# Optimization experiments

Measured on AMD Instinct MI355X. Metric: run time of the kernel, lower is better.

## Reference

```python
import jax, jax.numpy as jnp
import numpy as np

BATCH, SEQ_LEN, VEC_DIM, WIDTH = 64, 256, 512, 3


def setup_inputs() -> dict:
    key = jax.random.key(0)
    k = jax.random.split(key, 8)
    F0r = jax.random.normal(k[0], (BATCH, SEQ_LEN, VEC_DIM), jnp.float32)
    F1r = jax.random.normal(k[1], (BATCH, SEQ_LEN, VEC_DIM), jnp.float32)
    sent0_mask = (jax.random.uniform(k[2], (BATCH, SEQ_LEN)) < 0.9).astype(jnp.float32)
    sent1_mask = (jax.random.uniform(k[3], (BATCH, SEQ_LEN)) < 0.9).astype(jnp.float32)
    # nn.Parameter(torch.randn(seq_len, vec_dim))
    W0 = jax.random.normal(k[4], (SEQ_LEN, VEC_DIM), jnp.float32)
    W1 = jax.random.normal(k[5], (SEQ_LEN, VEC_DIM), jnp.float32)
    # Conv2d(2, 1, kernel_size=(WIDTH, 1)) default init: U(-1/sqrt(fan_in), +)
    bound = 1.0 / np.sqrt(2 * WIDTH * 1)
    conv_w = jax.random.uniform(k[6], (1, 2, WIDTH, 1), jnp.float32, -bound, bound)
    conv_b = jax.random.uniform(k[7], (1,), jnp.float32, -bound, bound)
    return dict(F0r=F0r, F1r=F1r, sent0_mask=sent0_mask, sent1_mask=sent1_mask,
                W0=W0, W1=W1, conv_w=conv_w, conv_b=conv_b)


def _conv_tanh_pool(x, conv_w, conv_b):
    # x: [B, 2, S, D]; conv pad (WIDTH-1, 0) -> [B, 1, S+WIDTH-1, D]
    y = jax.lax.conv_general_dilated(
        x, conv_w, window_strides=(1, 1),
        padding=((WIDTH - 1, WIDTH - 1), (0, 0)),
        dimension_numbers=('NCHW', 'OIHW', 'NCHW'))
    y = jnp.tanh(y + conv_b[None, :, None, None])
    # AvgPool2d kernel (WIDTH,1), stride 1 -> [B, 1, S, D]
    y = jax.lax.reduce_window(y, 0.0, jax.lax.add,
                              (1, 1, WIDTH, 1), (1, 1, 1, 1), 'VALID') / WIDTH
    return y[:, 0]  # squeeze channel -> [B, S, D]


def reference(F0r, F1r, sent0_mask, sent1_mask, W0, W1, conv_w, conv_b):
    # masking is in-place in the torch code, so masked F0/F1 feed the conv too
    F0 = F0r * sent0_mask[:, :, None]  # [B, S, D]
    F1 = F1r * sent1_mask[:, :, None]
    # pairwise L2 via ||u-v||^2 = ||u||^2 + ||v||^2 - 2 u.v (avoids [B,S,S,D])
    sq0 = jnp.sum(F0 * F0, axis=-1)  # [B, S]
    sq1 = jnp.sum(F1 * F1, axis=-1)
    cross = jnp.einsum('bid,bjd->bij', F0, F1)  # [B, S, S]
    d2 = jnp.maximum(sq0[:, :, None] + sq1[:, None, :] - 2.0 * cross, 0.0)
    norm = jnp.where(d2 > 0, jnp.sqrt(jnp.where(d2 > 0, d2, 1.0)), 0.0)
    A = 1.0 / (1.0 + norm)  # [B, S, S]
    F0a = jnp.einsum('bij,id->bjd', A, W0)  # A^T @ W0
    F1a = jnp.einsum('bij,jd->bid', A, W1)  # A @ W1
    x0 = jnp.stack([F0, F0a], axis=1)  # [B, 2, S, D]
    x1 = jnp.stack([F1, F1a], axis=1)
    out0 = _conv_tanh_pool(x0, conv_w, conv_b)
    out1 = _conv_tanh_pool(x1, conv_w, conv_b)
    return out0, out1
```

## Files before the change

kernel.cpp:

```cpp
#include <hip/hip_runtime.h>

typedef unsigned short u16;
typedef __attribute__((ext_vector_type(8))) short short8;
typedef __attribute__((ext_vector_type(4))) float f32x4;

__device__ inline u16 f2bf(float f) {
    union { float f; unsigned u; } v; v.f = f;
    unsigned u = v.u;
    unsigned r = (u + 0x7FFFu + ((u >> 16) & 1u)) >> 16;
    return (u16)r;
}
__device__ inline float bf2f(u16 h) {
    union { unsigned u; float f; } v; v.u = ((unsigned)h) << 16;
    return v.f;
}
__device__ inline float frcp(float x) { return __builtin_amdgcn_rcpf(x); }
__device__ inline float fsqrt(float x) { return __builtin_amdgcn_sqrtf(x); }
__device__ inline float ftanh(float x) {
    float e = __expf(2.f * x);
    return 1.f - 2.f * frcp(e + 1.f);
}
__device__ inline float4 bf4f(ushort4 u) {
    float4 f; f.x = bf2f(u.x); f.y = bf2f(u.y); f.z = bf2f(u.z); f.w = bf2f(u.w);
    return f;
}

typedef const __attribute__((address_space(1))) void* gas_ptr;
typedef __attribute__((address_space(3))) void* las_ptr;
__device__ __forceinline__ void gl2lds16(const u16* g, u16* l) {
    __builtin_amdgcn_global_load_lds((gas_ptr)(const void*)g, (las_ptr)(void*)l, 16, 0, 0);
}

__global__ __launch_bounds__(256) void prep_kernel(
    const float* __restrict__ F0r, const float* __restrict__ F1r,
    const float* __restrict__ m0, const float* __restrict__ m1,
    const float* __restrict__ W0, const float* __restrict__ W1,
    u16* __restrict__ F0b, u16* __restrict__ F1b,
    u16* __restrict__ WT0, u16* __restrict__ WT1,
    float* __restrict__ sq0, float* __restrict__ sq1)
{
    int bx = blockIdx.x;
    int t = threadIdx.x;
    if (bx >= 1024) {
        __shared__ u16 Wl[64][40];
        int idx2 = bx - 1024;
        int a = idx2 >> 6;
        int tile = idx2 & 63;
        int s0t = (tile >> 3) * 32, d0 = (tile & 7) * 64;
        const float* W = a ? W1 : W0;
        u16* WT = a ? WT1 : WT0;
        #pragma unroll
        for (int i = 0; i < 2; ++i) {
            int idx = i * 1024 + t * 4;
            int sl = idx >> 6, dl = idx & 63;
            float4 v = *(const float4*)(W + (size_t)(s0t + sl) * 512 + d0 + dl);
            Wl[dl + 0][sl] = f2bf(v.x);
            Wl[dl + 1][sl] = f2bf(v.y);
            Wl[dl + 2][sl] = f2bf(v.z);
            Wl[dl + 3][sl] = f2bf(v.w);
        }
        __syncthreads();
        #pragma unroll
        for (int i = 0; i < 2; ++i) {
            int idx = i * 1024 + t * 4;
            int dl = idx >> 5, sl = idx & 31;
            ushort4 v;
            v.x = Wl[dl][sl + 0]; v.y = Wl[dl][sl + 1];
            v.z = Wl[dl][sl + 2]; v.w = Wl[dl][sl + 3];
            *(ushort4*)(WT + (size_t)(d0 + dl) * 256 + s0t + sl) = v;
        }
        return;
    }
    int gw = (bx << 2) + (t >> 6);
    int lane = t & 63;
    for (int row = gw; row < 16384; row += 4096) {
        size_t base = (size_t)row * 512 + lane * 8;
        float mk0 = m0[row], mk1 = m1[row];
        float4 a0 = *(const float4*)(F0r + base);
        float4 a1 = *(const float4*)(F0r + base + 4);
        float4 b0 = *(const float4*)(F1r + base);
        float4 b1 = *(const float4*)(F1r + base + 4);
        a0.x *= mk0; a0.y *= mk0; a0.z *= mk0; a0.w *= mk0;
        a1.x *= mk0; a1.y *= mk0; a1.z *= mk0; a1.w *= mk0;
        b0.x *= mk1; b0.y *= mk1; b0.z *= mk1; b0.w *= mk1;
        b1.x *= mk1; b1.y *= mk1; b1.z *= mk1; b1.w *= mk1;
        ushort4 u0a, u0b, u1a, u1b;
        u0a.x = f2bf(a0.x); u0a.y = f2bf(a0.y); u0a.z = f2bf(a0.z); u0a.w = f2bf(a0.w);
        u0b.x = f2bf(a1.x); u0b.y = f2bf(a1.y); u0b.z = f2bf(a1.z); u0b.w = f2bf(a1.w);
        u1a.x = f2bf(b0.x); u1a.y = f2bf(b0.y); u1a.z = f2bf(b0.z); u1a.w = f2bf(b0.w);
        u1b.x = f2bf(b1.x); u1b.y = f2bf(b1.y); u1b.z = f2bf(b1.z); u1b.w = f2bf(b1.w);
        *(ushort4*)(F0b + base)     = u0a;
        *(ushort4*)(F0b + base + 4) = u0b;
        *(ushort4*)(F1b + base)     = u1a;
        *(ushort4*)(F1b + base + 4) = u1b;
        float s0p = a0.x*a0.x + a0.y*a0.y + a0.z*a0.z + a0.w*a0.w
                  + a1.x*a1.x + a1.y*a1.y + a1.z*a1.z + a1.w*a1.w;
        float s1p = b0.x*b0.x + b0.y*b0.y + b0.z*b0.z + b0.w*b0.w
                  + b1.x*b1.x + b1.y*b1.y + b1.z*b1.z + b1.w*b1.w;
        #pragma unroll
        for (int off = 32; off > 0; off >>= 1) {
            s0p += __shfl_xor(s0p, off);
            s1p += __shfl_xor(s1p, off);
        }
        if (lane == 0) { sq0[row] = s0p; sq1[row] = s1p; }
    }
}

__global__ __launch_bounds__(256) void fused_kernel(
    const u16* __restrict__ F0b, const u16* __restrict__ F1b,
    const float* __restrict__ sq0, const float* __restrict__ sq1,
    const u16* __restrict__ WT0, const u16* __restrict__ WT1,
    const float* __restrict__ cw, const float* __restrict__ cb,
    float* __restrict__ out)
{
    __shared__ __align__(16) u16 Al[36][264];
    __shared__ __align__(16) u16 region[21136];
    u16 (*Fl)[132] = (u16(*)[132])(region + 16384);

    int L = blockIdx.x + (blockIdx.y << 3) + (blockIdx.z << 9);
    int qq = L >> 6, rr = L & 63;
    int s0i = rr >> 3;
    int code = qq * 8 + (rr & 7);
    int b = code >> 1, side = code & 1;
    int s0 = s0i * 32;

    const u16* Sp  = (side ? F0b : F1b) + (size_t)b * 131072;
    const u16* Gp  = (side ? F1b : F0b) + (size_t)b * 131072;
    const float* sqS = (side ? sq0 : sq1) + b * 256;
    const float* sqG = (side ? sq1 : sq0) + b * 256;
    const u16* WT = side ? WT1 : WT0;
    const u16* Fb = (side ? F1b : F0b) + (size_t)b * 131072;
    float* o = out + (size_t)side * 8388608 + (size_t)b * 131072;

    const int t = threadIdx.x;
    const int lane = t & 63, w = t >> 6;
    const int q = lane >> 4, lm = lane & 15;

    f32x4 acc1[3][4];
    #pragma unroll
    for (int x = 0; x < 3; ++x)
        #pragma unroll
        for (int cn = 0; cn < 4; ++cn)
            acc1[x][cn] = (f32x4){0.f, 0.f, 0.f, 0.f};

    for (int kc = 0; kc < 512; kc += 64) {
        __syncthreads();
        #pragma unroll
        for (int i = 0; i < 8; ++i) {
            int idx = i * 256 + t;
            int r = idx >> 3, seg = idx & 7;
            int ss = seg ^ (r & 7);
            gl2lds16(Gp + (size_t)r * 512 + kc + ss * 8,
                     &region[(i * 256 + w * 64) * 8]);
        }
        {
            int idx = t;
            int r = idx >> 3, seg = idx & 7;
            int ss = seg ^ (r & 7);
            int s = s0 - 2 + r; s = s < 0 ? 0 : (s > 255 ? 255 : s);
            gl2lds16(Sp + (size_t)s * 512 + kc + ss * 8,
                     &region[16384 + (w * 64) * 8]);
        }
        if (t < 128) {
            int idx = 256 + t;
            int r = idx >> 3, seg = idx & 7;
            int ss = seg ^ (r & 7);
            int s = s0 - 2 + r; s = s < 0 ? 0 : (s > 255 ? 255 : s);
            gl2lds16(Sp + (size_t)s * 512 + kc + ss * 8,
                     &region[16384 + (256 + w * 64) * 8]);
        }
        __syncthreads();
        #pragma unroll
        for (int ks = 0; ks < 64; ks += 32) {
            int su = (((ks >> 3) + q) ^ (lm & 7)) * 8;
            short8 af[3], bfr[4];
            #pragma unroll
            for (int x = 0; x < 3; ++x)
                af[x] = *(const short8*)&region[16384 + (x * 16 + lm) * 64 + su];
            #pragma unroll
            for (int cn = 0; cn < 4; ++cn)
                bfr[cn] = *(const short8*)&region[(w * 64 + cn * 16 + lm) * 64 + su];
            #pragma unroll
            for (int x = 0; x < 3; ++x)
                #pragma unroll
                for (int cn = 0; cn < 4; ++cn)
                    acc1[x][cn] = __builtin_amdgcn_mfma_f32_16x16x32_bf16(
                        af[x], bfr[cn], acc1[x][cn], 0, 0, 0);
        }
    }
    __syncthreads();

    float sqg[4];
    #pragma unroll
    for (int cn = 0; cn < 4; ++cn) sqg[cn] = sqG[w * 64 + cn * 16 + lm];
    #pragma unroll
    for (int x = 0; x < 3; ++x) {
        #pragma unroll
        for (int r = 0; r < 4; ++r) {
            int m = x * 16 + q * 4 + r;
            if (m < 36) {
                int s = s0 - 2 + m;
                bool ok = (unsigned)s < 256u;
                float sqs = ok ? sqS[s] : 0.f;
                #pragma unroll
                for (int cn = 0; cn < 4; ++cn) {
                    float d2 = fmaxf(sqs + sqg[cn] - 2.f * acc1[x][cn][r], 0.f);
                    float a = ok ? frcp(1.f + fsqrt(d2)) : 0.f;
                    Al[m][w * 64 + cn * 16 + lm] = f2bf(a);
                }
            }
        }
    }

#define STAGE_B(bufo, nn, kb) do {                                             \
    _Pragma("unroll")                                                          \
    for (int i_ = 0; i_ < 4; ++i_) {                                           \
        int idx_ = i_ * 256 + t;                                               \
        int r_ = idx_ >> 3, seg_ = idx_ & 7;                                   \
        int ss_ = seg_ ^ (r_ & 7);                                             \
        gl2lds16(WT + (size_t)((nn) + r_) * 256 + (kb) + ss_ * 8,              \
                 &region[(bufo) + (i_ * 256 + w * 64) * 8]);                   \
    } } while (0)

    const u16* aRow[3];
    aRow[0] = &Al[lm][0];
    aRow[1] = &Al[16 + lm][0];
    aRow[2] = &Al[(lm < 4) ? (32 + lm) : 0][0];

    float w00 = cw[0], w01 = cw[1], w02 = cw[2];
    float w10 = cw[3], w11 = cw[4], w12 = cw[5];
    float bias = cb[0];
    const float third = 1.f / 3.f;
    const int g = t >> 5;
    const int dl = (t & 31) * 4;

    STAGE_B(0, 0, 0);

    for (int n0 = 0; n0 < 512; n0 += 128) {
        f32x4 acc[3][2];
        #pragma unroll
        for (int x = 0; x < 3; ++x)
            #pragma unroll
            for (int y = 0; y < 2; ++y)
                acc[x][y] = (f32x4){0.f, 0.f, 0.f, 0.f};

        #pragma unroll
        for (int kb_i = 0; kb_i < 4; ++kb_i) {
            __syncthreads();
            if (kb_i < 3)
                STAGE_B(((kb_i + 1) & 1) * 8192, n0, (kb_i + 1) * 64);
            const int cbuf = (kb_i & 1) * 8192;
            const int kb = kb_i * 64;
            #pragma unroll
            for (int ks = 0; ks < 64; ks += 32) {
                short8 af[3], bfr[2];
                #pragma unroll
                for (int x = 0; x < 3; ++x)
                    af[x] = *(const short8*)(aRow[x] + kb + ks + q * 8);
                #pragma unroll
                for (int y = 0; y < 2; ++y) {
                    int rb = w * 32 + y * 16 + lm;
                    int su = (((ks >> 3) + q) ^ (lm & 7)) * 8;
                    bfr[y] = *(const short8*)&region[cbuf + rb * 64 + su];
                }
                #pragma unroll
                for (int x = 0; x < 3; ++x)
                    #pragma unroll
                    for (int y = 0; y < 2; ++y)
                        acc[x][y] = __builtin_amdgcn_mfma_f32_16x16x32_bf16(
                            af[x], bfr[y], acc[x][y], 0, 0, 0);
            }
        }

        ushort4 frg[8];
        #pragma unroll
        for (int k = 0; k < 8; ++k) {
            int s = s0 + g * 4 - 2 + k;
            ushort4 z = {0, 0, 0, 0};
            frg[k] = ((unsigned)s < 256u)
                   ? *(const ushort4*)(Fb + (size_t)s * 512 + n0 + dl) : z;
        }

        #pragma unroll
        for (int x = 0; x < 3; ++x)
            #pragma unroll
            for (int r = 0; r < 4; ++r) {
                int m = x * 16 + q * 4 + r;
                if (m < 36) {
                    #pragma unroll
                    for (int y = 0; y < 2; ++y)
                        Fl[m][w * 32 + y * 16 + lm] = f2bf(acc[x][y][r]);
                }
            }
        __syncthreads();

        if (n0 < 384)
            STAGE_B(0, n0 + 128, 0);

        float4 f[8], a[8];
        #pragma unroll
        for (int k = 0; k < 8; ++k) {
            f[k] = bf4f(frg[k]);
            a[k] = bf4f(*(const ushort4*)&Fl[g * 4 + k][dl]);
        }
        float4 ty[6];
        #pragma unroll
        for (int k = 0; k < 6; ++k) {
            float4 y;
            y.x = bias + w00*f[k].x + w01*f[k+1].x + w02*f[k+2].x + w10*a[k].x + w11*a[k+1].x + w12*a[k+2].x;
            y.y = bias + w00*f[k].y + w01*f[k+1].y + w02*f[k+2].y + w10*a[k].y + w11*a[k+1].y + w12*a[k+2].y;
            y.z = bias + w00*f[k].z + w01*f[k+1].z + w02*f[k+2].z + w10*a[k].z + w11*a[k+1].z + w12*a[k+2].z;
            y.w = bias + w00*f[k].w + w01*f[k+1].w + w02*f[k+2].w + w10*a[k].w + w11*a[k+1].w + w12*a[k+2].w;
            y.x = ftanh(y.x); y.y = ftanh(y.y); y.z = ftanh(y.z); y.w = ftanh(y.w);
            ty[k] = y;
        }
        #pragma unroll
        for (int r = 0; r < 4; ++r) {
            float4 res;
            res.x = (ty[r].x + ty[r+1].x + ty[r+2].x) * third;
            res.y = (ty[r].y + ty[r+1].y + ty[r+2].y) * third;
            res.z = (ty[r].z + ty[r+1].z + ty[r+2].z) * third;
            res.w = (ty[r].w + ty[r+1].w + ty[r+2].w) * third;
            *(float4*)(o + (size_t)(s0 + g * 4 + r) * 512 + n0 + dl) = res;
        }
    }
#undef STAGE_B
}

extern "C" void kernel_launch(void* const* d_in, const int* in_sizes, int n_in,
                              void* d_out, int out_size, void* d_ws, size_t ws_size,
                              hipStream_t stream)
{
    const float* F0r = (const float*)d_in[0];
    const float* F1r = (const float*)d_in[1];
    const float* m0  = (const float*)d_in[2];
    const float* m1  = (const float*)d_in[3];
    const float* W0  = (const float*)d_in[4];
    const float* W1  = (const float*)d_in[5];
    const float* cw  = (const float*)d_in[6];
    const float* cb  = (const float*)d_in[7];
    float* out = (float*)d_out;

    char* ws = (char*)d_ws;
    u16* F0b   = (u16*)(ws);
    u16* F1b   = (u16*)(ws + 16777216);
    float* sq0 = (float*)(ws + 50331648);
    float* sq1 = (float*)(ws + 50397184);
    u16* WT0   = (u16*)(ws + 50462720);
    u16* WT1   = (u16*)(ws + 50724864);

    prep_kernel<<<1152, 256, 0, stream>>>(F0r, F1r, m0, m1, W0, W1,
                                          F0b, F1b, WT0, WT1, sq0, sq1);
    fused_kernel<<<dim3(8, 64, 2), 256, 0, stream>>>(F0b, F1b, sq0, sq1,
                                                     WT0, WT1, cw, cb, out);
}
```

Measured before the change: 188.9 us.

## Fuse masking, bf16 conversion and row norms into the main kernel

Removes the prep pass that wrote masked bf16 copies of F0/F1 and their squared norms. The fused kernel now reads fp32 inputs directly, masks and converts them in registers, and stages the bf16 tiles into LDS. Row norms are accumulated in shared memory, and global loads for the next chunk are software-prefetched into registers. This saves a round trip of intermediate tensors through HBM, but the fused kernel reads fp32 data, twice as many bytes, and each block re-reads the full G matrix. Register pressure also goes up.

```diff
diff --git a/kernel.cpp b/kernel.cpp
--- a/kernel.cpp
+++ b/kernel.cpp
@@ -14,6 +14,9 @@
     union { unsigned u; float f; } v; v.u = ((unsigned)h) << 16;
     return v.f;
 }
+__device__ inline unsigned pack2(float lo, float hi) {
+    return (unsigned)f2bf(lo) | ((unsigned)f2bf(hi) << 16);
+}
 __device__ inline float frcp(float x) { return __builtin_amdgcn_rcpf(x); }
 __device__ inline float fsqrt(float x) { return __builtin_amdgcn_sqrtf(x); }
 __device__ inline float ftanh(float x) {
@@ -31,90 +34,51 @@
     __builtin_amdgcn_global_load_lds((gas_ptr)(const void*)g, (las_ptr)(void*)l, 16, 0, 0);
 }
 
-__global__ __launch_bounds__(256) void prep_kernel(
+__global__ __launch_bounds__(256) void wtrans_kernel(
+    const float* __restrict__ W0, const float* __restrict__ W1,
+    u16* __restrict__ WT0, u16* __restrict__ WT1)
+{
+    __shared__ u16 Wl[64][40];
+    int idx2 = blockIdx.x;
+    int a = idx2 >> 6;
+    int tile = idx2 & 63;
+    int s0t = (tile >> 3) * 32, d0 = (tile & 7) * 64;
+    const float* W = a ? W1 : W0;
+    u16* WT = a ? WT1 : WT0;
+    int t = threadIdx.x;
+    #pragma unroll
+    for (int i = 0; i < 2; ++i) {
+        int idx = i * 1024 + t * 4;
+        int sl = idx >> 6, dl = idx & 63;
+        float4 v = *(const float4*)(W + (size_t)(s0t + sl) * 512 + d0 + dl);
+        Wl[dl + 0][sl] = f2bf(v.x);
+        Wl[dl + 1][sl] = f2bf(v.y);
+        Wl[dl + 2][sl] = f2bf(v.z);
+        Wl[dl + 3][sl] = f2bf(v.w);
+    }
+    __syncthreads();
+    #pragma unroll
+    for (int i = 0; i < 2; ++i) {
+        int idx = i * 1024 + t * 4;
+        int dl = idx >> 5, sl = idx & 31;
+        ushort4 v;
+        v.x = Wl[dl][sl + 0]; v.y = Wl[dl][sl + 1];
+        v.z = Wl[dl][sl + 2]; v.w = Wl[dl][sl + 3];
+        *(ushort4*)(WT + (size_t)(d0 + dl) * 256 + s0t + sl) = v;
+    }
+}
+
+__global__ __launch_bounds__(256) void fused_kernel(
     const float* __restrict__ F0r, const float* __restrict__ F1r,
     const float* __restrict__ m0, const float* __restrict__ m1,
-    const float* __restrict__ W0, const float* __restrict__ W1,
-    u16* __restrict__ F0b, u16* __restrict__ F1b,
-    u16* __restrict__ WT0, u16* __restrict__ WT1,
-    float* __restrict__ sq0, float* __restrict__ sq1)
-{
-    int bx = blockIdx.x;
-    int t = threadIdx.x;
-    if (bx >= 1024) {
-        __shared__ u16 Wl[64][40];
-        int idx2 = bx - 1024;
-        int a = idx2 >> 6;
-        int tile = idx2 & 63;
-        int s0t = (tile >> 3) * 32, d0 = (tile & 7) * 64;
-        const float* W = a ? W1 : W0;
-        u16* WT = a ? WT1 : WT0;
-        #pragma unroll
-        for (int i = 0; i < 2; ++i) {
-            int idx = i * 1024 + t * 4;
-            int sl = idx >> 6, dl = idx & 63;
-            float4 v = *(const float4*)(W + (size_t)(s0t + sl) * 512 + d0 + dl);
-            Wl[dl + 0][sl] = f2bf(v.x);
-            Wl[dl + 1][sl] = f2bf(v.y);
-            Wl[dl + 2][sl] = f2bf(v.z);
-            Wl[dl + 3][sl] = f2bf(v.w);
-        }
-        __syncthreads();
-        #pragma unroll
-        for (int i = 0; i < 2; ++i) {
-            int idx = i * 1024 + t * 4;
-            int dl = idx >> 5, sl = idx & 31;
-            ushort4 v;
-            v.x = Wl[dl][sl + 0]; v.y = Wl[dl][sl + 1];
-            v.z = Wl[dl][sl + 2]; v.w = Wl[dl][sl + 3];
-            *(ushort4*)(WT + (size_t)(d0 + dl) * 256 + s0t + sl) = v;
-        }
-        return;
-    }
-    int gw = (bx << 2) + (t >> 6);
-    int lane = t & 63;
-    for (int row = gw; row < 16384; row += 4096) {
-        size_t base = (size_t)row * 512 + lane * 8;
-        float mk0 = m0[row], mk1 = m1[row];
-        float4 a0 = *(const float4*)(F0r + base);
-        float4 a1 = *(const float4*)(F0r + base + 4);
-        float4 b0 = *(const float4*)(F1r + base);
-        float4 b1 = *(const float4*)(F1r + base + 4);
-        a0.x *= mk0; a0.y *= mk0; a0.z *= mk0; a0.w *= mk0;
-        a1.x *= mk0; a1.y *= mk0; a1.z *= mk0; a1.w *= mk0;
-        b0.x *= mk1; b0.y *= mk1; b0.z *= mk1; b0.w *= mk1;
-        b1.x *= mk1; b1.y *= mk1; b1.z *= mk1; b1.w *= mk1;
-        ushort4 u0a, u0b, u1a, u1b;
-        u0a.x = f2bf(a0.x); u0a.y = f2bf(a0.y); u0a.z = f2bf(a0.z); u0a.w = f2bf(a0.w);
-        u0b.x = f2bf(a1.x); u0b.y = f2bf(a1.y); u0b.z = f2bf(a1.z); u0b.w = f2bf(a1.w);
-        u1a.x = f2bf(b0.x); u1a.y = f2bf(b0.y); u1a.z = f2bf(b0.z); u1a.w = f2bf(b0.w);
-        u1b.x = f2bf(b1.x); u1b.y = f2bf(b1.y); u1b.z = f2bf(b1.z); u1b.w = f2bf(b1.w);
-        *(ushort4*)(F0b + base)     = u0a;
-        *(ushort4*)(F0b + base + 4) = u0b;
-        *(ushort4*)(F1b + base)     = u1a;
-        *(ushort4*)(F1b + base + 4) = u1b;
-        float s0p = a0.x*a0.x + a0.y*a0.y + a0.z*a0.z + a0.w*a0.w
-                  + a1.x*a1.x + a1.y*a1.y + a1.z*a1.z + a1.w*a1.w;
-        float s1p = b0.x*b0.x + b0.y*b0.y + b0.z*b0.z + b0.w*b0.w
-                  + b1.x*b1.x + b1.y*b1.y + b1.z*b1.z + b1.w*b1.w;
-        #pragma unroll
-        for (int off = 32; off > 0; off >>= 1) {
-            s0p += __shfl_xor(s0p, off);
-            s1p += __shfl_xor(s1p, off);
-        }
-        if (lane == 0) { sq0[row] = s0p; sq1[row] = s1p; }
-    }
-}
-
-__global__ __launch_bounds__(256) void fused_kernel(
-    const u16* __restrict__ F0b, const u16* __restrict__ F1b,
-    const float* __restrict__ sq0, const float* __restrict__ sq1,
     const u16* __restrict__ WT0, const u16* __restrict__ WT1,
     const float* __restrict__ cw, const float* __restrict__ cb,
     float* __restrict__ out)
 {
     __shared__ __align__(16) u16 Al[36][264];
     __shared__ __align__(16) u16 region[21136];
+    __shared__ float sqG_l[256];
+    __shared__ float sqS_l[48];
     u16 (*Fl)[132] = (u16(*)[132])(region + 16384);
 
     int L = blockIdx.x + (blockIdx.y << 3) + (blockIdx.z << 9);
@@ -124,17 +88,29 @@
     int b = code >> 1, side = code & 1;
     int s0 = s0i * 32;
 
-    const u16* Sp  = (side ? F0b : F1b) + (size_t)b * 131072;
-    const u16* Gp  = (side ? F1b : F0b) + (size_t)b * 131072;
-    const float* sqS = (side ? sq0 : sq1) + b * 256;
-    const float* sqG = (side ? sq1 : sq0) + b * 256;
+    const float* Gf = (side ? F1r : F0r) + (size_t)b * 131072;
+    const float* Sf = (side ? F0r : F1r) + (size_t)b * 131072;
+    const float* mg = (side ? m1 : m0) + b * 256;
+    const float* ms = (side ? m0 : m1) + b * 256;
     const u16* WT = side ? WT1 : WT0;
-    const u16* Fb = (side ? F1b : F0b) + (size_t)b * 131072;
     float* o = out + (size_t)side * 8388608 + (size_t)b * 131072;
 
     const int t = threadIdx.x;
     const int lane = t & 63, w = t >> 6;
     const int q = lane >> 4, lm = lane & 15;
+    const int seg = t & 7, rbase = t >> 3;
+
+    float mGr[8];
+    #pragma unroll
+    for (int i = 0; i < 8; ++i) mGr[i] = mg[rbase + i * 32];
+    int rs1 = 32 + rbase;
+    int cs0 = s0 - 2 + rbase; cs0 = cs0 < 0 ? 0 : (cs0 > 255 ? 255 : cs0);
+    int cs1 = s0 - 2 + rs1;   cs1 = cs1 < 0 ? 0 : (cs1 > 255 ? 255 : cs1);
+    float mS0 = ms[cs0];
+    float mS1 = (t < 128) ? ms[cs1] : 0.f;
+
+    sqG_l[t] = 0.f;
+    if (t < 48) sqS_l[t] = 0.f;
 
     f32x4 acc1[3][4];
     #pragma unroll
@@ -143,33 +119,50 @@
         for (int cn = 0; cn < 4; ++cn)
             acc1[x][cn] = (f32x4){0.f, 0.f, 0.f, 0.f};
 
-    for (int kc = 0; kc < 512; kc += 64) {
+    float4 gA[16], gS[4];
+#define PH1_LOAD(kc) do {                                                      \
+    _Pragma("unroll")                                                          \
+    for (int i_ = 0; i_ < 8; ++i_) {                                           \
+        const float* p_ = Gf + (size_t)(rbase + i_ * 32) * 512 + (kc) + seg * 8; \
+        gA[2*i_]   = *(const float4*)p_;                                       \
+        gA[2*i_+1] = *(const float4*)(p_ + 4);                                 \
+    }                                                                          \
+    { const float* p_ = Sf + (size_t)cs0 * 512 + (kc) + seg * 8;               \
+      gS[0] = *(const float4*)p_; gS[1] = *(const float4*)(p_ + 4); }          \
+    if (t < 128) {                                                             \
+      const float* p_ = Sf + (size_t)cs1 * 512 + (kc) + seg * 8;               \
+      gS[2] = *(const float4*)p_; gS[3] = *(const float4*)(p_ + 4); }          \
+  } while (0)
+
+#define STAGE1(va, vb, mm, rr_, base_, sql_) do {                              \
+    float4 a_ = va, d_ = vb; float m_ = mm;                                    \
+    a_.x*=m_; a_.y*=m_; a_.z*=m_; a_.w*=m_;                                    \
+    d_.x*=m_; d_.y*=m_; d_.z*=m_; d_.w*=m_;                                    \
+    float ss_ = a_.x*a_.x + a_.y*a_.y + a_.z*a_.z + a_.w*a_.w                  \
+              + d_.x*d_.x + d_.y*d_.y + d_.z*d_.z + d_.w*d_.w;                 \
+    ss_ += __shfl_xor(ss_, 1); ss_ += __shfl_xor(ss_, 2); ss_ += __shfl_xor(ss_, 4); \
+    uint4 u_;                                                                  \
+    u_.x = pack2(a_.x, a_.y); u_.y = pack2(a_.z, a_.w);                        \
+    u_.z = pack2(d_.x, d_.y); u_.w = pack2(d_.z, d_.w);                        \
+    *(uint4*)&region[(base_) + (rr_) * 64 + (seg ^ ((rr_) & 7)) * 8] = u_;     \
+    if (seg == 0) sql_[rr_] += ss_;                                            \
+  } while (0)
+
+    PH1_LOAD(0);
+
+    for (int c = 0; c < 8; ++c) {
         __syncthreads();
         #pragma unroll
         for (int i = 0; i < 8; ++i) {
-            int idx = i * 256 + t;
-            int r = idx >> 3, seg = idx & 7;
-            int ss = seg ^ (r & 7);
-            gl2lds16(Gp + (size_t)r * 512 + kc + ss * 8,
-                     &region[(i * 256 + w * 64) * 8]);
-        }
-        {
-            int idx = t;
-            int r = idx >> 3, seg = idx & 7;
-            int ss = seg ^ (r & 7);
-            int s = s0 - 2 + r; s = s < 0 ? 0 : (s > 255 ? 255 : s);
-            gl2lds16(Sp + (size_t)s * 512 + kc + ss * 8,
-                     &region[16384 + (w * 64) * 8]);
-        }
-        if (t < 128) {
-            int idx = 256 + t;
-            int r = idx >> 3, seg = idx & 7;
-            int ss = seg ^ (r & 7);
-            int s = s0 - 2 + r; s = s < 0 ? 0 : (s > 255 ? 255 : s);
-            gl2lds16(Sp + (size_t)s * 512 + kc + ss * 8,
-                     &region[16384 + (256 + w * 64) * 8]);
-        }
-        __syncthreads();
+            int r = rbase + i * 32;
+            STAGE1(gA[2*i], gA[2*i+1], mGr[i], r, 0, sqG_l);
+        }
+        STAGE1(gS[0], gS[1], mS0, rbase, 16384, sqS_l);
+        if (t < 128)
+            STAGE1(gS[2], gS[3], mS1, rs1, 16384, sqS_l);
+        if (c < 7) PH1_LOAD((c + 1) * 64);
+        asm volatile("s_waitcnt lgkmcnt(0)" ::: "memory");
+        __builtin_amdgcn_s_barrier();
         #pragma unroll
         for (int ks = 0; ks < 64; ks += 32) {
             int su = (((ks >> 3) + q) ^ (lm & 7)) * 8;
@@ -189,10 +182,9 @@
         }
     }
     __syncthreads();
-
-    float sqg[4];
-    #pragma unroll
-    for (int cn = 0; cn < 4; ++cn) sqg[cn] = sqG[w * 64 + cn * 16 + lm];
+#undef PH1_LOAD
+#undef STAGE1
+
     #pragma unroll
     for (int x = 0; x < 3; ++x) {
         #pragma unroll
@@ -201,12 +193,13 @@
             if (m < 36) {
                 int s = s0 - 2 + m;
                 bool ok = (unsigned)s < 256u;
-                float sqs = ok ? sqS[s] : 0.f;
+                float sqs = sqS_l[m];
                 #pragma unroll
                 for (int cn = 0; cn < 4; ++cn) {
-                    float d2 = fmaxf(sqs + sqg[cn] - 2.f * acc1[x][cn][r], 0.f);
+                    int j = w * 64 + cn * 16 + lm;
+                    float d2 = fmaxf(sqs + sqG_l[j] - 2.f * acc1[x][cn][r], 0.f);
                     float a = ok ? frcp(1.f + fsqrt(d2)) : 0.f;
-                    Al[m][w * 64 + cn * 16 + lm] = f2bf(a);
+                    Al[m][j] = f2bf(a);
                 }
             }
         }
@@ -234,6 +227,15 @@
     const int g = t >> 5;
     const int dl = (t & 31) * 4;
 
+    float mF[8]; int csF[8];
+    #pragma unroll
+    for (int k = 0; k < 8; ++k) {
+        int s = s0 + g * 4 - 2 + k;
+        bool ok = (unsigned)s < 256u;
+        csF[k] = ok ? s : 0;
+        mF[k] = ok ? mg[s] : 0.f;
+    }
+
     STAGE_B(0, 0, 0);
 
     for (int n0 = 0; n0 < 512; n0 += 128) {
@@ -272,14 +274,10 @@
             }
         }
 
-        ushort4 frg[8];
-        #pragma unroll
-        for (int k = 0; k < 8; ++k) {
-            int s = s0 + g * 4 - 2 + k;
-            ushort4 z = {0, 0, 0, 0};
-            frg[k] = ((unsigned)s < 256u)
-                   ? *(const ushort4*)(Fb + (size_t)s * 512 + n0 + dl) : z;
-        }
+        float4 frg[8];
+        #pragma unroll
+        for (int k = 0; k < 8; ++k)
+            frg[k] = *(const float4*)(Gf + (size_t)csF[k] * 512 + n0 + dl);
 
         #pragma unroll
         for (int x = 0; x < 3; ++x)
@@ -300,7 +298,8 @@
         float4 f[8], a[8];
         #pragma unroll
         for (int k = 0; k < 8; ++k) {
-            f[k] = bf4f(frg[k]);
+            f[k].x = frg[k].x * mF[k]; f[k].y = frg[k].y * mF[k];
+            f[k].z = frg[k].z * mF[k]; f[k].w = frg[k].w * mF[k];
             a[k] = bf4f(*(const ushort4*)&Fl[g * 4 + k][dl]);
         }
         float4 ty[6];
@@ -342,15 +341,10 @@
     float* out = (float*)d_out;
 
     char* ws = (char*)d_ws;
-    u16* F0b   = (u16*)(ws);
-    u16* F1b   = (u16*)(ws + 16777216);
-    float* sq0 = (float*)(ws + 50331648);
-    float* sq1 = (float*)(ws + 50397184);
-    u16* WT0   = (u16*)(ws + 50462720);
-    u16* WT1   = (u16*)(ws + 50724864);
-
-    prep_kernel<<<1152, 256, 0, stream>>>(F0r, F1r, m0, m1, W0, W1,
-                                          F0b, F1b, WT0, WT1, sq0, sq1);
-    fused_kernel<<<dim3(8, 64, 2), 256, 0, stream>>>(F0b, F1b, sq0, sq1,
+    u16* WT0 = (u16*)(ws);
+    u16* WT1 = (u16*)(ws + 262144);
+
+    wtrans_kernel<<<128, 256, 0, stream>>>(W0, W1, WT0, WT1);
+    fused_kernel<<<dim3(8, 64, 2), 256, 0, stream>>>(F0r, F1r, m0, m1,
                                                      WT0, WT1, cw, cb, out);
 }
```

Result: slower. 210.0 us (+11.2%).
